# Kernel optimization log

Measured on AMD Instinct MI355X. Metric: run time of the kernel, lower is better.

## Reference

```python
import jax, jax.numpy as jnp
import numpy as np

N = 100_000
E = 3_200_000
P = 128
K = 128


def setup_inputs() -> dict:
    key = jax.random.key(0)
    ks = jax.random.split(key, 12)

    def xavier(k, shape):
        fan_in, fan_out = shape[1], shape[0]
        lim = jnp.sqrt(6.0 / (fan_in + fan_out))
        return jax.random.uniform(k, shape, jnp.float32, -lim, lim)

    return {
        "s_v": jax.random.normal(ks[0], (N,), jnp.float32),
        "t_v": jax.random.normal(ks[1], (N,), jnp.float32),
        "x": jax.random.normal(ks[2], (N, K), jnp.float32),
        "edge_src": jax.random.randint(ks[3], (E,), 0, N),
        "edge_dst": jax.random.randint(ks[4], (E,), 0, N),
        "theta1": xavier(ks[5], (P, 2)),
        "theta2": xavier(ks[6], (P, K)),
        "theta3": xavier(ks[7], (2 * P, 1)),
        "theta4": xavier(ks[8], (P, P)),
        "theta5": xavier(ks[9], (P, P)),
        "h_theta": xavier(ks[10], (P, 2 * P)),
    }


def reference(s_v, t_v, x, edge_src, edge_dst, theta1, theta2, theta3, theta4, theta5, h_theta):
    n = x.shape[0]
    # per-node embedding: mu_v = relu(theta1 @ conn + theta2 @ x_v_normalized)
    conn = jnp.stack([s_v, t_v], axis=1)                      # [N, 2]
    norm = jnp.linalg.norm(x, axis=1, keepdims=True)          # [N, 1]
    xn = x / jnp.where(norm == 0, 1.0, norm)
    mu = jax.nn.relu(conn @ theta1.T + xn @ theta2.T)         # [N, P]
    # neighbor-difference sum: s_v = deg(v)*mu_v - sum_{u in N(v)} mu_u
    ones = jnp.ones(edge_src.shape, mu.dtype)
    deg = jax.ops.segment_sum(ones, edge_src, num_segments=n)           # [N]
    nb_sum = jax.ops.segment_sum(mu[edge_dst], edge_src, num_segments=n)  # [N, P]
    s = deg[:, None] * mu - nb_sum
    # mu' = h_theta @ relu([mu; s])
    mu_prime = jax.nn.relu(jnp.concatenate([mu, s], axis=1)) @ h_theta.T  # [N, P]
    sum_mu_prime = mu_prime.sum(axis=0)                        # [P]
    # Q_v = theta3^T relu([theta4 @ sum_mu'; theta5 @ mu'_v])
    up = theta4 @ sum_mu_prime                                 # [P], shared
    down = mu_prime @ theta5.T                                 # [N, P]
    z = jax.nn.relu(jnp.concatenate([jnp.broadcast_to(up, (n, up.shape[0])), down], axis=1))
    return z @ theta3                                          # [N, 1]
```

## Files before the change

### kernel.cpp

```cpp
#include <hip/hip_runtime.h>
#include <stdint.h>

typedef unsigned int uint;
typedef unsigned short ushort;
typedef __attribute__((ext_vector_type(4))) float f32x4;
typedef __attribute__((ext_vector_type(2))) float f32x2;
typedef __attribute__((ext_vector_type(8))) short bf16x8;

union U4H8 { uint4 u; bf16x8 h; };

__device__ __forceinline__ float bflo(uint u){ return __uint_as_float(u << 16); }
__device__ __forceinline__ float bfhi(uint u){ return __uint_as_float(u & 0xffff0000u); }
__device__ __forceinline__ ushort f2bf(float f){
  uint u = __float_as_uint(f);
  return (ushort)((u + 0x7fffu + ((u >> 16) & 1u)) >> 16);
}
__device__ __forceinline__ uint pack2(float lo, float hi){
  return ((uint)f2bf(hi) << 16) | (uint)f2bf(lo);
}

__device__ __forceinline__ uint fp8e(float f){
  uint u = __float_as_uint(f);
  uint r = u + 0x7FFFFu + ((u >> 20) & 1u);
  uint code = (((r >> 23) - 120u) << 3) | ((r >> 20) & 7u);
  code = (code > 0x7Eu) ? 0x7Eu : code;
  uint den = (uint)__float2int_rn(f * 512.0f);
  return (f >= 0.015625f) ? code : den;
}

__device__ __forceinline__ void fp8acc(float* acc, uint w, int off){
  f32x2 lo = __builtin_amdgcn_cvt_pk_f32_fp8(w, false);
  f32x2 hi = __builtin_amdgcn_cvt_pk_f32_fp8(w, true);
  acc[off+0] += lo[0]; acc[off+1] += lo[1];
  acc[off+2] += hi[0]; acc[off+3] += hi[1];
}

#define CHUNK 8192
#define GGRID 2048
#define REDB  64

__global__ __launch_bounds__(256) void k_mu(
    const float* __restrict__ x, const float* __restrict__ sv,
    const float* __restrict__ tv, const float* __restrict__ th1,
    const float* __restrict__ th2, ushort* __restrict__ mu_s,
    uint2* __restrict__ mu8, int n)
{
  __shared__ uint4 B[2048];
  const int tid = threadIdx.x;
  for (int f = tid; f < 2048; f += 256) {
    int l = f & 63, rest = f >> 6;
    int s = rest >> 3, t = rest & 7;
    int row = t*16 + (l & 15);
    int kb  = s*32 + (l >> 4)*8;
    const float* p = th2 + row*128 + kb;
    float4 a = *(const float4*)p;
    float4 b = *(const float4*)(p + 4);
    uint4 u; u.x = pack2(a.x,a.y); u.y = pack2(a.z,a.w);
    u.z = pack2(b.x,b.y); u.w = pack2(b.z,b.w);
    B[(s*8 + t)*64 + l] = u;
  }
  __syncthreads();
  const int w = tid >> 6, l = tid & 63, q = l >> 4, c = l & 15;
  float2 t1[8];
  #pragma unroll
  for (int t = 0; t < 8; ++t) t1[t] = ((const float2*)th1)[t*16 + c];
  const int ntiles = (n + 15) >> 4;
  for (int T = blockIdx.x*4 + w; T < ntiles; T += gridDim.x*4) {
    int v0 = T*16;
    int arow = min(v0 + c, n-1);
    const float4* xr = (const float4*)(x + (size_t)arow*128);
    float4 xf[8];
    #pragma unroll
    for (int s = 0; s < 4; ++s) {
      xf[2*s]   = xr[s*8 + q*2];
      xf[2*s+1] = xr[s*8 + q*2 + 1];
    }
    float ss = 0.f;
    #pragma unroll
    for (int i = 0; i < 8; ++i)
      ss += xf[i].x*xf[i].x + xf[i].y*xf[i].y + xf[i].z*xf[i].z + xf[i].w*xf[i].w;
    ss += __shfl_xor(ss, 16, 64);
    ss += __shfl_xor(ss, 32, 64);
    float inv = (ss > 0.f) ? rsqrtf(ss) : 1.f;
    U4H8 a[4];
    #pragma unroll
    for (int s = 0; s < 4; ++s) {
      float4 u0 = xf[2*s], u1 = xf[2*s+1];
      a[s].u = make_uint4(pack2(u0.x*inv, u0.y*inv), pack2(u0.z*inv, u0.w*inv),
                          pack2(u1.x*inv, u1.y*inv), pack2(u1.z*inv, u1.w*inv));
    }
    f32x4 acc[8];
    #pragma unroll
    for (int t = 0; t < 8; ++t) acc[t] = (f32x4){0.f,0.f,0.f,0.f};
    #pragma unroll
    for (int s = 0; s < 4; ++s) {
      #pragma unroll
      for (int t = 0; t < 8; ++t) {
        U4H8 b; b.u = B[(s*8 + t)*64 + l];
        acc[t] = __builtin_amdgcn_mfma_f32_16x16x32_bf16(a[s].h, b.h, acc[t], 0, 0, 0);
      }
    }
    float svr[4], tvr[4];
    #pragma unroll
    for (int r = 0; r < 4; ++r) {
      int node = min(v0 + q*4 + r, n-1);
      svr[r] = sv[node]; tvr[r] = tv[node];
    }
    #pragma unroll
    for (int r = 0; r < 4; ++r) {
      int node = v0 + q*4 + r;
      if (node < n) {
        float mm[8];
        #pragma unroll
        for (int t = 0; t < 8; ++t) {
          mm[t] = fmaxf(acc[t][r] + t1[t].x*svr[r] + t1[t].y*tvr[r], 0.f);
          mu_s[(size_t)node*128 + t*16 + c] = f2bf(mm[t]);
        }
        uint u0 = fp8e(mm[0]) | (fp8e(mm[1]) << 8) |
                  (fp8e(mm[2]) << 16) | (fp8e(mm[3]) << 24);
        uint u1 = fp8e(mm[4]) | (fp8e(mm[5]) << 8) |
                  (fp8e(mm[6]) << 16) | (fp8e(mm[7]) << 24);
        mu8[(size_t)node*16 + c] = make_uint2(u0, u1);
      }
    }
  }
}

__global__ __launch_bounds__(256) void k_m2(const float* __restrict__ th5,
    const float* __restrict__ hth, float* __restrict__ M2)
{
  __shared__ float row[128];
  const int r = blockIdx.x, j = threadIdx.x;
  if (j < 128) row[j] = th5[r*128 + j];
  __syncthreads();
  float acc = 0.f;
  #pragma unroll 8
  for (int k = 0; k < 128; ++k) acc += row[k] * hth[k*256 + j];
  M2[r*256 + j] = acc;
}


__global__ __launch_bounds__(512) void k_hist(const int* __restrict__ src,
    int* __restrict__ histG, int e, int nblk)
{
  __shared__ int lh[256];
  const int blk = blockIdx.x, tid = threadIdx.x;
  if (tid < 256) lh[tid] = 0;
  __syncthreads();
  const int lo = blk*CHUNK, hi = min(e, lo + CHUNK);
  for (int i = lo + tid; i < hi; i += 512)
    atomicAdd(&lh[src[i] >> 9], 1);
  __syncthreads();
  if (tid < 256) histG[tid*nblk + blk] = lh[tid];
}

__global__ __launch_bounds__(512) void k_scanH(int* __restrict__ histG,
    int* __restrict__ bucketTot, int nblk)
{
  __shared__ int tmp[512];
  const int b = blockIdx.x, tid = threadIdx.x;
  int v = (tid < nblk) ? histG[b*nblk + tid] : 0;
  tmp[tid] = v; __syncthreads();
  for (int off = 1; off < 512; off <<= 1) {
    int t = (tid >= off) ? tmp[tid - off] : 0;
    __syncthreads();
    tmp[tid] += t;
    __syncthreads();
  }
  if (tid < nblk) histG[b*nblk + tid] = tmp[tid] - v;
  if (tid == nblk - 1) bucketTot[b] = tmp[tid];
}

__global__ __launch_bounds__(256) void k_scanB(const int* __restrict__ bucketTot,
    int* __restrict__ bucketBase)
{
  __shared__ int tmp[256];
  int tid = threadIdx.x;
  int v = bucketTot[tid];
  tmp[tid] = v; __syncthreads();
  for (int off = 1; off < 256; off <<= 1) {
    int t = (tid >= off) ? tmp[tid - off] : 0;
    __syncthreads();
    tmp[tid] += t;
    __syncthreads();
  }
  bucketBase[tid] = tmp[tid] - v;
}

__global__ __launch_bounds__(512) void k_part(
    const int* __restrict__ src, const int* __restrict__ dst,
    const int* __restrict__ histG, const int* __restrict__ bucketBase,
    uint* __restrict__ packed, int e, int nblk)
{
  __shared__ int cur[256];
  const int blk = blockIdx.x, tid = threadIdx.x;
  if (tid < 256) cur[tid] = bucketBase[tid] + histG[tid*nblk + blk];
  __syncthreads();
  const int lo = blk*CHUNK, hi = min(e, lo + CHUNK);
  for (int i = lo + tid; i < hi; i += 512) {
    int s = src[i], d = dst[i];
    int pos = atomicAdd(&cur[s >> 9], 1);
    packed[pos] = ((uint)(s & 511) << 17) | (uint)d;
  }
}

__global__ __launch_bounds__(512) void k_csr(
    const uint* __restrict__ packed, const int* __restrict__ bucketTot,
    const int* __restrict__ bucketBase, int* __restrict__ sorted,
    int* __restrict__ rowstart, int* __restrict__ cnt, int n)
{
  __shared__ int lc[512];
  __shared__ int lofs[512];
  __shared__ int lcur[512];
  const int b = blockIdx.x, tid = threadIdx.x;
  const int base = bucketBase[b], tot = bucketTot[b];
  lc[tid] = 0; __syncthreads();
  for (int i = tid; i < tot; i += 512)
    atomicAdd(&lc[packed[base + i] >> 17], 1);
  __syncthreads();
  lofs[tid] = lc[tid]; __syncthreads();
  for (int off = 1; off < 512; off <<= 1) {
    int t = (tid >= off) ? lofs[tid - off] : 0;
    __syncthreads();
    lofs[tid] += t;
    __syncthreads();
  }
  int excl = lofs[tid] - lc[tid];
  int node = (b << 9) + tid;
  lcur[tid] = base + excl;
  if (node < n) { rowstart[node] = base + excl; cnt[node] = lc[tid]; }
  __syncthreads();
  for (int i = tid; i < tot; i += 512) {
    uint p = packed[base + i];
    int pos = atomicAdd(&lcur[p >> 17], 1);
    sorted[pos] = (int)(p & 0x1FFFFu);
  }
}

__global__ __launch_bounds__(256) void k_gather(
    const uint4* __restrict__ mu8, const uint* __restrict__ mu_u,
    const int* __restrict__ sorted, const int* __restrict__ cnt,
    const int* __restrict__ rowstart, uint* __restrict__ rs_u,
    float* __restrict__ part, int n)
{
  __shared__ float ls[4*256];
  const int w = threadIdx.x >> 6, l = threadIdx.x & 63;
  const int g = l >> 3, c = l & 7;
  float cm0 = 0.f, cm1 = 0.f, cr0 = 0.f, cr1 = 0.f;
  for (int v = blockIdx.x*4 + w; v < n; v += gridDim.x*4) {
    int deg = cnt[v], start = rowstart[v];
    float acc[16];
    #pragma unroll
    for (int i = 0; i < 16; ++i) acc[i] = 0.f;
    for (int base = 0; base < deg; base += 64) {
      int m = min(deg - base, 64);
      int idx = (l < m) ? sorted[start + base + l] : 0;
      int full = m & ~7;
      for (int j = 0; j < full; j += 8) {
        int d = __shfl(idx, j + g, 64);
        uint4 u = mu8[(size_t)d*8 + c];
        fp8acc(acc, u.x, 0); fp8acc(acc, u.y, 4);
        fp8acc(acc, u.z, 8); fp8acc(acc, u.w, 12);
      }
      int rem = m - full;
      if (rem) {
        int d = __shfl(idx, full + min(g, rem-1), 64);
        if (g < rem) {
          uint4 u = mu8[(size_t)d*8 + c];
          fp8acc(acc, u.x, 0); fp8acc(acc, u.y, 4);
          fp8acc(acc, u.z, 8); fp8acc(acc, u.w, 12);
        }
      }
    }
    uint um = mu_u[(size_t)v*64 + l];
    #pragma unroll
    for (int i = 0; i < 16; ++i) {
      acc[i] += __shfl_xor(acc[i], 8, 64);
      acc[i] += __shfl_xor(acc[i], 16, 64);
      acc[i] += __shfl_xor(acc[i], 32, 64);
    }
    float a01 = (g & 1) ? acc[1] : acc[0];
    float a23 = (g & 1) ? acc[3] : acc[2];
    float a45 = (g & 1) ? acc[5] : acc[4];
    float a67 = (g & 1) ? acc[7] : acc[6];
    float b01 = (g & 1) ? acc[9]  : acc[8];
    float b23 = (g & 1) ? acc[11] : acc[10];
    float b45 = (g & 1) ? acc[13] : acc[12];
    float b67 = (g & 1) ? acc[15] : acc[14];
    float a03 = (g & 2) ? a23 : a01;
    float a47 = (g & 2) ? a67 : a45;
    float b03 = (g & 2) ? b23 : b01;
    float b47 = (g & 2) ? b67 : b45;
    float alo = (g & 4) ? a47 : a03;
    float ahi = (g & 4) ? b47 : b03;
    float m0 = bflo(um), m1 = bfhi(um);
    float dg = (float)deg;
    float s0 = fmaxf(dg*m0 - alo, 0.f);
    float s1 = fmaxf(dg*m1 - ahi, 0.f);
    rs_u[(size_t)v*64 + l] = pack2(s0, s1);
    cm0 += m0; cm1 += m1;
    cr0 += s0; cr1 += s1;
  }
  ls[w*256 + 2*l]         = cm0;
  ls[w*256 + 2*l + 1]     = cm1;
  ls[w*256 + 128 + 2*l]   = cr0;
  ls[w*256 + 128 + 2*l+1] = cr1;
  __syncthreads();
  int tid = threadIdx.x;
  part[(size_t)blockIdx.x*256 + tid] =
      ls[tid] + ls[256+tid] + ls[512+tid] + ls[768+tid];
}

__global__ __launch_bounds__(256) void k_red(const float* __restrict__ part,
    float* __restrict__ part2)
{
  const int t = threadIdx.x, b = blockIdx.x;
  const int rpb = GGRID / REDB;
  float s = 0.f;
  for (int r = b*rpb; r < b*rpb + rpb; ++r) s += part[(size_t)r*256 + t];
  part2[(size_t)b*256 + t] = s;
}

__global__ __launch_bounds__(128) void k_upC(const float* __restrict__ part,
    int npart, const float* __restrict__ hth, const float* __restrict__ th4,
    const float* __restrict__ th3, float* __restrict__ Cbuf) {
  __shared__ float Q[256];
  __shared__ float S[128];
  __shared__ float pr[128];
  int tid = threadIdx.x;
  float q0 = 0.f, q1 = 0.f;
  for (int b = 0; b < npart; ++b) {
    q0 += part[(size_t)b*256 + tid];
    q1 += part[(size_t)b*256 + 128 + tid];
  }
  Q[tid] = q0; Q[128 + tid] = q1;
  __syncthreads();
  float gs = 0.f;
  const float4* hr = (const float4*)(hth + tid*256);
  const float4* Q4 = (const float4*)Q;
  #pragma unroll 8
  for (int k = 0; k < 64; ++k) {
    float4 a = hr[k], b = Q4[k];
    gs += a.x*b.x + a.y*b.y + a.z*b.z + a.w*b.w;
  }
  S[tid] = gs;
  __syncthreads();
  float up = 0.f;
  const float4* r4 = (const float4*)(th4 + tid*128);
  const float4* S4 = (const float4*)S;
  #pragma unroll 8
  for (int k = 0; k < 32; ++k) {
    float4 a = r4[k], b = S4[k];
    up += a.x*b.x + a.y*b.y + a.z*b.z + a.w*b.w;
  }
  float r = th3[tid] * fmaxf(up, 0.f);
  pr[tid] = r; __syncthreads();
  if (tid < 64) pr[tid] += pr[tid + 64];
  __syncthreads();
  if (tid < 64) {
    float v = pr[tid];
    #pragma unroll
    for (int off = 32; off > 0; off >>= 1) v += __shfl_down(v, off, 64);
    if (tid == 0) Cbuf[0] = v;
  }
}

__global__ __launch_bounds__(256) void k_out(
    const uint4* __restrict__ mu4, const uint4* __restrict__ rs4,
    const float* __restrict__ M2, const float* __restrict__ th3,
    const float* __restrict__ Cbuf, float* __restrict__ out, int n)
{
  __shared__ uint4 B[4096];
  const int tid = threadIdx.x;
  for (int f = tid; f < 4096; f += 256) {
    int l = f & 63, rest = f >> 6;
    int s = rest >> 3, t = rest & 7;
    int row = t*16 + (l & 15);
    int kb  = s*32 + (l >> 4)*8;
    const float* p = M2 + row*256 + kb;
    float4 a = *(const float4*)p;
    float4 b = *(const float4*)(p + 4);
    uint4 u; u.x = pack2(a.x,a.y); u.y = pack2(a.z,a.w);
    u.z = pack2(b.x,b.y); u.w = pack2(b.z,b.w);
    B[(s*8 + t)*64 + l] = u;
  }
  __syncthreads();
  const int w = tid >> 6, l = tid & 63, q = l >> 4, c = l & 15;
  float t3w[8];
  #pragma unroll
  for (int t = 0; t < 8; ++t) t3w[t] = th3[128 + t*16 + c];
  const float C = Cbuf[0];
  const int ntiles = (n + 15) >> 4;
  for (int T = blockIdx.x*4 + w; T < ntiles; T += gridDim.x*4) {
    int v0 = T*16;
    int arow = min(v0 + c, n-1);
    U4H8 a[8];
    #pragma unroll
    for (int s = 0; s < 4; ++s) a[s].u   = mu4[(size_t)arow*16 + s*4 + q];
    #pragma unroll
    for (int s = 0; s < 4; ++s) a[4+s].u = rs4[(size_t)arow*16 + s*4 + q];
    f32x4 acc[8];
    #pragma unroll
    for (int t = 0; t < 8; ++t) acc[t] = (f32x4){0.f,0.f,0.f,0.f};
    #pragma unroll
    for (int s = 0; s < 8; ++s) {
      #pragma unroll
      for (int t = 0; t < 8; ++t) {
        U4H8 b; b.u = B[(s*8 + t)*64 + l];
        acc[t] = __builtin_amdgcn_mfma_f32_16x16x32_bf16(a[s].h, b.h, acc[t], 0, 0, 0);
      }
    }
    float red[4] = {0.f, 0.f, 0.f, 0.f};
    #pragma unroll
    for (int t = 0; t < 8; ++t) {
      #pragma unroll
      for (int r = 0; r < 4; ++r)
        red[r] += t3w[t] * fmaxf(acc[t][r], 0.f);
    }
    #pragma unroll
    for (int r = 0; r < 4; ++r) {
      #pragma unroll
      for (int off = 1; off < 16; off <<= 1)
        red[r] += __shfl_xor(red[r], off, 64);
    }
    if (c == 0) {
      #pragma unroll
      for (int r = 0; r < 4; ++r) {
        int node = v0 + q*4 + r;
        if (node < n) out[node] = C + red[r];
      }
    }
  }
}

extern "C" void kernel_launch(void* const* d_in, const int* in_sizes, int n_in,
                              void* d_out, int out_size, void* d_ws, size_t ws_size,
                              hipStream_t stream)
{
  const float* sv  = (const float*)d_in[0];
  const float* tv  = (const float*)d_in[1];
  const float* x   = (const float*)d_in[2];
  const int*   esrc= (const int*)d_in[3];
  const int*   edst= (const int*)d_in[4];
  const float* th1 = (const float*)d_in[5];
  const float* th2 = (const float*)d_in[6];
  const float* th3 = (const float*)d_in[7];
  const float* th4 = (const float*)d_in[8];
  const float* th5 = (const float*)d_in[9];
  const float* hth = (const float*)d_in[10];
  float* out = (float*)d_out;
  const int n = in_sizes[0];
  const int e = in_sizes[3];

  const int nblk  = (e + CHUNK - 1) / CHUNK;
  const int nbuck = (n + 511) >> 9;

  char* wp = (char*)d_ws;
  auto carve = [&](size_t bytes) { char* p = wp; wp += (bytes + 255) & ~(size_t)255; return p; };
  char*   R1    = (char*) carve((size_t)n*128*2);
  ushort* mu_s  = (ushort*)carve((size_t)n*128*2);
  ushort* rs_s  = (ushort*)carve((size_t)n*128*2);
  int*    sorted= (int*)   carve((size_t)e*4);
  int*    cnt   = (int*)   carve((size_t)n*4);
  int*    rowst = (int*)   carve((size_t)n*4);
  int*    histG = (int*)   carve((size_t)256*nblk*4);
  int*    btot  = (int*)   carve(256*4);
  int*    bbase = (int*)   carve(256*4);
  float*  M2    = (float*) carve(128*256*4);
  float*  part  = (float*) carve((size_t)GGRID*256*4);
  float*  part2 = (float*) carve((size_t)REDB*256*4);
  float*  Cbuf  = (float*) carve(256);

  uint*   packed= (uint*)R1;
  uint2*  mu8   = (uint2*)(R1 + (size_t)n*128);

  k_mu    <<<1024, 256, 0, stream>>>(x, sv, tv, th1, th2, mu_s, mu8, n);
  k_m2    <<<128, 256, 0, stream>>>(th5, hth, M2);
  k_hist  <<<nblk, 512, 0, stream>>>(esrc, histG, e, nblk);
  k_scanH <<<256, 512, 0, stream>>>(histG, btot, nblk);
  k_scanB <<<1, 256, 0, stream>>>(btot, bbase);
  k_part  <<<nblk, 512, 0, stream>>>(esrc, edst, histG, bbase, packed, e, nblk);
  k_csr   <<<nbuck, 512, 0, stream>>>(packed, btot, bbase, sorted, rowst, cnt, n);
  k_gather<<<GGRID, 256, 0, stream>>>((const uint4*)mu8, (const uint*)mu_s,
                                      sorted, cnt, rowst, (uint*)rs_s, part, n);
  k_red   <<<REDB, 256, 0, stream>>>(part, part2);
  k_upC   <<<1, 128, 0, stream>>>(part2, REDB, hth, th4, th3, Cbuf);
  k_out   <<<1024, 256, 0, stream>>>((const uint4*)mu_s, (const uint4*)rs_s,
                                     M2, th3, Cbuf, out, n);
}
```

Before: 369.7 us.

## Merge histogram and M2 kernels into mu kernel via block-role dispatch

```diff
diff --git a/kernel.cpp b/kernel.cpp
--- a/kernel.cpp
+++ b/kernel.cpp
@@ -36,6 +36,7 @@
 }
 
 #define CHUNK 8192
+#define NB_MU 1024
 #define GGRID 2048
 #define REDB  64
 
@@ -43,10 +44,38 @@
     const float* __restrict__ x, const float* __restrict__ sv,
     const float* __restrict__ tv, const float* __restrict__ th1,
     const float* __restrict__ th2, ushort* __restrict__ mu_s,
-    uint2* __restrict__ mu8, int n)
+    uint2* __restrict__ mu8, int n,
+    const int* __restrict__ esrc, int* __restrict__ histG, int e, int nblk,
+    const float* __restrict__ th5, const float* __restrict__ hth,
+    float* __restrict__ M2)
 {
   __shared__ uint4 B[2048];
+  __shared__ int lh[256];
+  __shared__ float m2row[128];
   const int tid = threadIdx.x;
+  const int bid = blockIdx.x;
+
+  if (bid >= NB_MU) {
+    if (bid < NB_MU + nblk) {
+      const int blk = bid - NB_MU;
+      lh[tid] = 0; __syncthreads();
+      const int lo = blk*CHUNK, hi = min(e, lo + CHUNK);
+      for (int i = lo + tid; i < hi; i += 256)
+        atomicAdd(&lh[esrc[i] >> 9], 1);
+      __syncthreads();
+      histG[tid*nblk + blk] = lh[tid];
+    } else {
+      const int r = bid - NB_MU - nblk;
+      if (tid < 128) m2row[tid] = th5[r*128 + tid];
+      __syncthreads();
+      float accv = 0.f;
+      #pragma unroll 8
+      for (int k = 0; k < 128; ++k) accv += m2row[k] * hth[k*256 + tid];
+      M2[r*256 + tid] = accv;
+    }
+    return;
+  }
+
   for (int f = tid; f < 2048; f += 256) {
     int l = f & 63, rest = f >> 6;
     int s = rest >> 3, t = rest & 7;
@@ -65,7 +94,7 @@
   #pragma unroll
   for (int t = 0; t < 8; ++t) t1[t] = ((const float2*)th1)[t*16 + c];
   const int ntiles = (n + 15) >> 4;
-  for (int T = blockIdx.x*4 + w; T < ntiles; T += gridDim.x*4) {
+  for (int T = bid*4 + w; T < ntiles; T += NB_MU*4) {
     int v0 = T*16;
     int arow = min(v0 + c, n-1);
     const float4* xr = (const float4*)(x + (size_t)arow*128);
@@ -126,33 +155,6 @@
   }
 }
 
-__global__ __launch_bounds__(256) void k_m2(const float* __restrict__ th5,
-    const float* __restrict__ hth, float* __restrict__ M2)
-{
-  __shared__ float row[128];
-  const int r = blockIdx.x, j = threadIdx.x;
-  if (j < 128) row[j] = th5[r*128 + j];
-  __syncthreads();
-  float acc = 0.f;
-  #pragma unroll 8
-  for (int k = 0; k < 128; ++k) acc += row[k] * hth[k*256 + j];
-  M2[r*256 + j] = acc;
-}
-
-
-__global__ __launch_bounds__(512) void k_hist(const int* __restrict__ src,
-    int* __restrict__ histG, int e, int nblk)
-{
-  __shared__ int lh[256];
-  const int blk = blockIdx.x, tid = threadIdx.x;
-  if (tid < 256) lh[tid] = 0;
-  __syncthreads();
-  const int lo = blk*CHUNK, hi = min(e, lo + CHUNK);
-  for (int i = lo + tid; i < hi; i += 512)
-    atomicAdd(&lh[src[i] >> 9], 1);
-  __syncthreads();
-  if (tid < 256) histG[tid*nblk + blk] = lh[tid];
-}
 
 __global__ __launch_bounds__(512) void k_scanH(int* __restrict__ histG,
     int* __restrict__ bucketTot, int nblk)
@@ -474,9 +476,9 @@
   uint*   packed= (uint*)R1;
   uint2*  mu8   = (uint2*)(R1 + (size_t)n*128);
 
-  k_mu    <<<1024, 256, 0, stream>>>(x, sv, tv, th1, th2, mu_s, mu8, n);
-  k_m2    <<<128, 256, 0, stream>>>(th5, hth, M2);
-  k_hist  <<<nblk, 512, 0, stream>>>(esrc, histG, e, nblk);
+  k_mu    <<<NB_MU + nblk + 128, 256, 0, stream>>>(x, sv, tv, th1, th2, mu_s,
+                                                   mu8, n, esrc, histG, e, nblk,
+                                                   th5, hth, M2);
   k_scanH <<<256, 512, 0, stream>>>(histG, btot, nblk);
   k_scanB <<<1, 256, 0, stream>>>(btot, bbase);
   k_part  <<<nblk, 512, 0, stream>>>(esrc, edst, histG, bbase, packed, e, nblk);
```

New measurement: 362.7 us. No clear change (-1.9%).
